# Kernel tuning notes

Measured on AMD Instinct MI355X. Metric: run time of the kernel, lower is better.

## Reference

```python
import jax, jax.numpy as jnp
import numpy as np

N_DOMAIN, D_IN, UNITS, LORA_R = 64, 256, 128, 4
BATCH = 131072


def setup_inputs() -> dict:
    key = jax.random.key(0)
    ks = jax.random.split(key, 7)
    x = jax.random.normal(ks[0], (BATCH, D_IN), dtype=jnp.float32)
    domain_indicator = jax.random.randint(ks[1], (BATCH, 1), 0, N_DOMAIN, dtype=jnp.int32)
    a_kernel = jax.random.normal(ks[2], (N_DOMAIN, D_IN, LORA_R), dtype=jnp.float32) * 0.05
    b_kernel = jax.random.normal(ks[3], (N_DOMAIN, LORA_R, UNITS), dtype=jnp.float32) * 0.05
    domain_bias = jax.random.normal(ks[4], (N_DOMAIN, UNITS), dtype=jnp.float32) * 0.05
    kernel = jax.random.normal(ks[5], (D_IN, UNITS), dtype=jnp.float32) * 0.05
    bias = jax.random.normal(ks[6], (UNITS,), dtype=jnp.float32) * 0.05
    return {"x": x, "domain_indicator": domain_indicator, "a_kernel": a_kernel,
            "b_kernel": b_kernel, "domain_bias": domain_bias, "kernel": kernel, "bias": bias}


def reference(x, domain_indicator, a_kernel, b_kernel, domain_bias, kernel, bias):
    # shared dense path (dropout is identity at inference)
    out = x @ kernel + bias  # [B, units]
    # domain index: original uses domain_indicator[0, 0] (one domain per batch)
    idx = domain_indicator[0, 0]
    A = a_kernel[idx]        # [d_in, r]
    B = b_kernel[idx]        # [r, units]
    db = domain_bias[idx]    # [units]
    out = out + (x @ A) @ B + db
    return jax.nn.relu(out)
```

## Files before the change

kernel.cpp:

```cpp
#include <hip/hip_runtime.h>
#include <hip/hip_bf16.h>

#define D_IN   256
#define UNITS  128
#define LORA_R 4
#define GRID_GEMM 8192

typedef __attribute__((ext_vector_type(8))) short short8;
typedef __attribute__((ext_vector_type(4))) float f32x4;

static __device__ __forceinline__ unsigned short f2bf(float f) {
    unsigned u = __float_as_uint(f);
    unsigned r = (u + 0x7FFFu + ((u >> 16) & 1u)) >> 16;
    return (unsigned short)r;
}

static __device__ __forceinline__ void gll16(const void* g, void* l) {
    __builtin_amdgcn_global_load_lds(
        (const __attribute__((address_space(1))) unsigned int*)g,
        (__attribute__((address_space(3))) unsigned int*)l,
        16, 0, 0);
}

__global__ void mlora_prep(const float* __restrict__ a_kernel,
                           const float* __restrict__ b_kernel,
                           const float* __restrict__ domain_bias,
                           const float* __restrict__ kernel,
                           const float* __restrict__ bias,
                           const int* __restrict__ dom,
                           unsigned short* __restrict__ wfrag,
                           float* __restrict__ bias_eff) {
    const int idx = dom[0];
    const int tid = blockIdx.x * 256 + threadIdx.x;
    const int n = tid & (UNITS - 1);
    const int k = tid >> 7;
    const float* __restrict__ A = a_kernel + (size_t)idx * D_IN * LORA_R;
    const float* __restrict__ B = b_kernel + (size_t)idx * LORA_R * UNITS;
    float w = kernel[k * UNITS + n];
#pragma unroll
    for (int r = 0; r < LORA_R; ++r) w += A[k * LORA_R + r] * B[r * UNITS + n];
    const int s = k >> 5, g = (k >> 3) & 3, j = k & 7;
    const int t = n >> 4, lo = n & 15;
    const int lane = g * 16 + lo;
    wfrag[(size_t)((s * 8 + t) * 64 + lane) * 8 + j] = f2bf(w);
    if (tid < UNITS) bias_eff[tid] = bias[tid] + domain_bias[idx * UNITS + tid];
}

__global__ __launch_bounds__(256, 5) void mlora_gemm(
    const float* __restrict__ x,
    const unsigned short* __restrict__ wfrag,
    const float* __restrict__ bias_eff,
    float* __restrict__ out) {
    __shared__ float lds[16 * 256];
    const int lane = threadIdx.x & 63;
    const int wave = threadIdx.x >> 6;
    const int t0 = wave * 2;
    const int rlo = lane & 15;
    const int g = lane >> 4;

    short8 bfrag[8][2];
#pragma unroll
    for (int s = 0; s < 8; ++s) {
#pragma unroll
        for (int tt = 0; tt < 2; ++tt) {
            bfrag[s][tt] = *reinterpret_cast<const short8*>(
                wfrag + (size_t)((s * 8 + t0 + tt) * 64 + lane) * 8);
        }
    }
    const float b0 = bias_eff[t0 * 16 + rlo];
    const float b1 = bias_eff[(t0 + 1) * 16 + rlo];

    const size_t row0 = (size_t)blockIdx.x * 16;
    const char* gbase = (const char*)x + (row0 + wave * 4) * 1024;
    char* lbase = (char*)lds + (size_t)wave * 4 * 1024;
#pragma unroll
    for (int i = 0; i < 4; ++i) {
        const int rsw = (wave * 4 + i) & 7;
        gll16(gbase + (size_t)i * 1024 + ((lane * 16) ^ (rsw << 4)),
              lbase + (size_t)i * 1024);
    }
    __syncthreads();

    const int swz = (rlo & 7) << 4;
    const char* lrow = (const char*)lds + (size_t)rlo * 1024;
    f32x4 acc0 = {0.f, 0.f, 0.f, 0.f};
    f32x4 acc1 = {0.f, 0.f, 0.f, 0.f};
#pragma unroll
    for (int s = 0; s < 8; ++s) {
        const int base = s * 128 + g * 32;
        f32x4 u0 = *reinterpret_cast<const f32x4*>(lrow + (base ^ swz));
        f32x4 u1 = *reinterpret_cast<const f32x4*>(lrow + ((base + 16) ^ swz));
        union { short8 s8; __hip_bfloat162 h2[4]; } af;
        af.h2[0] = __float22bfloat162_rn(make_float2(u0[0], u0[1]));
        af.h2[1] = __float22bfloat162_rn(make_float2(u0[2], u0[3]));
        af.h2[2] = __float22bfloat162_rn(make_float2(u1[0], u1[1]));
        af.h2[3] = __float22bfloat162_rn(make_float2(u1[2], u1[3]));
        acc0 = __builtin_amdgcn_mfma_f32_16x16x32_bf16(af.s8, bfrag[s][0], acc0, 0, 0, 0);
        acc1 = __builtin_amdgcn_mfma_f32_16x16x32_bf16(af.s8, bfrag[s][1], acc1, 0, 0, 0);
    }
    float* op = out + (row0 + g * 4) * UNITS;
#pragma unroll
    for (int j = 0; j < 4; ++j) {
        op[(size_t)j * UNITS + t0 * 16 + rlo]      = fmaxf(acc0[j] + b0, 0.f);
        op[(size_t)j * UNITS + t0 * 16 + 16 + rlo] = fmaxf(acc1[j] + b1, 0.f);
    }
}

extern "C" void kernel_launch(void* const* d_in, const int* in_sizes, int n_in,
                              void* d_out, int out_size, void* d_ws, size_t ws_size,
                              hipStream_t stream) {
    const float* x           = (const float*)d_in[0];
    const int*   dom         = (const int*)d_in[1];
    const float* a_kernel    = (const float*)d_in[2];
    const float* b_kernel    = (const float*)d_in[3];
    const float* domain_bias = (const float*)d_in[4];
    const float* kernel      = (const float*)d_in[5];
    const float* bias        = (const float*)d_in[6];
    float* out = (float*)d_out;

    unsigned short* wfrag = (unsigned short*)d_ws;
    float* bias_eff = (float*)((char*)d_ws + 65536);

    mlora_prep<<<128, 256, 0, stream>>>(a_kernel, b_kernel, domain_bias,
                                        kernel, bias, dom, wfrag, bias_eff);
    mlora_gemm<<<GRID_GEMM, 256, 0, stream>>>(x, wfrag, bias_eff, out);
}
```

Before: 44.92 us.

## Process four row tiles per block with double-buffered LDS prefetch

Each GEMM block now handles four 16-row tiles instead of one, so the grid is cut by four. The block keeps two LDS buffers: the next tile's x rows are loaded with global_load_lds while the current tile is computed, and hand-placed s_waitcnt vmcnt counts plus s_barrier order the loads and stores. This spreads the per-block weight-fragment register loads over more rows and hides x load latency behind MFMA work. The cost is lower occupancy from the launch bound of 4 and double LDS use, plus fragile hand-counted vmcnt values that depend on how the compiler orders memory operations.

New measurement: 40.63 us. -9.6%, faster.

```diff
diff --git a/kernel.cpp b/kernel.cpp
--- a/kernel.cpp
+++ b/kernel.cpp
@@ -4,10 +4,15 @@
 #define D_IN   256
 #define UNITS  128
 #define LORA_R 4
-#define GRID_GEMM 8192
+#define ROWS_PER_TILE   16
+#define TILES_PER_BLOCK 4
+#define GRID_GEMM       2048
 
 typedef __attribute__((ext_vector_type(8))) short short8;
 typedef __attribute__((ext_vector_type(4))) float f32x4;
+
+#define BARRIER()  asm volatile("s_barrier" ::: "memory")
+#define VMCNT(n)   asm volatile("s_waitcnt vmcnt(" #n ")" ::: "memory")
 
 static __device__ __forceinline__ unsigned short f2bf(float f) {
     unsigned u = __float_as_uint(f);
@@ -46,12 +51,12 @@
     if (tid < UNITS) bias_eff[tid] = bias[tid] + domain_bias[idx * UNITS + tid];
 }
 
-__global__ __launch_bounds__(256, 5) void mlora_gemm(
+__global__ __launch_bounds__(256, 4) void mlora_gemm(
     const float* __restrict__ x,
     const unsigned short* __restrict__ wfrag,
     const float* __restrict__ bias_eff,
     float* __restrict__ out) {
-    __shared__ float lds[16 * 256];
+    __shared__ float lds[2][ROWS_PER_TILE * 256];
     const int lane = threadIdx.x & 63;
     const int wave = threadIdx.x >> 6;
     const int t0 = wave * 2;
@@ -70,40 +75,67 @@
     const float b0 = bias_eff[t0 * 16 + rlo];
     const float b1 = bias_eff[(t0 + 1) * 16 + rlo];
 
-    const size_t row0 = (size_t)blockIdx.x * 16;
-    const char* gbase = (const char*)x + (row0 + wave * 4) * 1024;
-    char* lbase = (char*)lds + (size_t)wave * 4 * 1024;
+    const size_t block_row0 = (size_t)blockIdx.x * (ROWS_PER_TILE * TILES_PER_BLOCK);
+    const int swz = (rlo & 7) << 4;
+
+    auto stage = [&](int bufi, int tile) {
+        const char* gbase = (const char*)x +
+            (block_row0 + (size_t)tile * ROWS_PER_TILE + wave * 4) * 1024;
+        char* lbase = (char*)&lds[bufi][0] + (size_t)wave * 4 * 1024;
 #pragma unroll
-    for (int i = 0; i < 4; ++i) {
-        const int rsw = (wave * 4 + i) & 7;
-        gll16(gbase + (size_t)i * 1024 + ((lane * 16) ^ (rsw << 4)),
-              lbase + (size_t)i * 1024);
-    }
-    __syncthreads();
+        for (int i = 0; i < 4; ++i) {
+            const int rsw = (wave * 4 + i) & 7;
+            gll16(gbase + (size_t)i * 1024 + ((lane * 16) ^ (rsw << 4)),
+                  lbase + (size_t)i * 1024);
+        }
+    };
 
-    const int swz = (rlo & 7) << 4;
-    const char* lrow = (const char*)lds + (size_t)rlo * 1024;
-    f32x4 acc0 = {0.f, 0.f, 0.f, 0.f};
-    f32x4 acc1 = {0.f, 0.f, 0.f, 0.f};
+    auto compute_tile = [&](int bufi, int tile) {
+        const size_t r0g = block_row0 + (size_t)tile * ROWS_PER_TILE;
+        const char* lrow = (const char*)&lds[bufi][0] + (size_t)rlo * 1024;
+        f32x4 acc0 = {0.f, 0.f, 0.f, 0.f};
+        f32x4 acc1 = {0.f, 0.f, 0.f, 0.f};
 #pragma unroll
-    for (int s = 0; s < 8; ++s) {
-        const int base = s * 128 + g * 32;
-        f32x4 u0 = *reinterpret_cast<const f32x4*>(lrow + (base ^ swz));
-        f32x4 u1 = *reinterpret_cast<const f32x4*>(lrow + ((base + 16) ^ swz));
-        union { short8 s8; __hip_bfloat162 h2[4]; } af;
-        af.h2[0] = __float22bfloat162_rn(make_float2(u0[0], u0[1]));
-        af.h2[1] = __float22bfloat162_rn(make_float2(u0[2], u0[3]));
-        af.h2[2] = __float22bfloat162_rn(make_float2(u1[0], u1[1]));
-        af.h2[3] = __float22bfloat162_rn(make_float2(u1[2], u1[3]));
-        acc0 = __builtin_amdgcn_mfma_f32_16x16x32_bf16(af.s8, bfrag[s][0], acc0, 0, 0, 0);
-        acc1 = __builtin_amdgcn_mfma_f32_16x16x32_bf16(af.s8, bfrag[s][1], acc1, 0, 0, 0);
-    }
-    float* op = out + (row0 + g * 4) * UNITS;
+        for (int s = 0; s < 8; ++s) {
+            const int base = s * 128 + g * 32;
+            f32x4 u0 = *reinterpret_cast<const f32x4*>(lrow + (base ^ swz));
+            f32x4 u1 = *reinterpret_cast<const f32x4*>(lrow + ((base + 16) ^ swz));
+            union { short8 s8; __hip_bfloat162 h2[4]; } af;
+            af.h2[0] = __float22bfloat162_rn(make_float2(u0[0], u0[1]));
+            af.h2[1] = __float22bfloat162_rn(make_float2(u0[2], u0[3]));
+            af.h2[2] = __float22bfloat162_rn(make_float2(u1[0], u1[1]));
+            af.h2[3] = __float22bfloat162_rn(make_float2(u1[2], u1[3]));
+            acc0 = __builtin_amdgcn_mfma_f32_16x16x32_bf16(af.s8, bfrag[s][0], acc0, 0, 0, 0);
+            acc1 = __builtin_amdgcn_mfma_f32_16x16x32_bf16(af.s8, bfrag[s][1], acc1, 0, 0, 0);
+        }
+        float* op = out + (r0g + g * 4) * UNITS;
 #pragma unroll
-    for (int j = 0; j < 4; ++j) {
-        op[(size_t)j * UNITS + t0 * 16 + rlo]      = fmaxf(acc0[j] + b0, 0.f);
-        op[(size_t)j * UNITS + t0 * 16 + 16 + rlo] = fmaxf(acc1[j] + b1, 0.f);
-    }
+        for (int j = 0; j < 4; ++j) {
+            op[(size_t)j * UNITS + t0 * 16 + rlo]      = fmaxf(acc0[j] + b0, 0.f);
+            op[(size_t)j * UNITS + t0 * 16 + 16 + rlo] = fmaxf(acc1[j] + b1, 0.f);
+        }
+    };
+
+    stage(0, 0);
+
+    stage(1, 1);
+    VMCNT(4);
+    BARRIER();
+    compute_tile(0, 0);
+    BARRIER();
+    stage(0, 2);
+    VMCNT(12);
+    BARRIER();
+    compute_tile(1, 1);
+    BARRIER();
+    stage(1, 3);
+    VMCNT(12);
+    BARRIER();
+    compute_tile(0, 2);
+    BARRIER();
+    VMCNT(8);
+    BARRIER();
+    compute_tile(1, 3);
 }
 
 extern "C" void kernel_launch(void* const* d_in, const int* in_sizes, int n_in,
```
